# Kernel optimization log

Measured on AMD Instinct MI355X. Metric: run time of the kernel, lower is better.

Reference implementation:

```python
import jax, jax.numpy as jnp
import numpy as np

B, C, T = 32, 512, 2048
OUT_SEQ_LEN = 80
SIGMA2 = 10.0


def setup_inputs() -> dict:
    key = jax.random.key(0)
    k1, k2, k3, k4, k5, k6 = jax.random.split(key, 6)
    x = jax.random.normal(k1, (B, C, T), dtype=jnp.float32)
    # lengths in [T//2, T], with at least one equal to T (torch broadcast assumes max(len)==T)
    len_fea = jax.random.randint(k2, (B,), T // 2, T + 1)
    len_fea = len_fea.at[0].set(T)
    s1 = 1.0 / np.sqrt(C)
    conv1_w = jax.random.uniform(k3, (C, C), jnp.float32, -s1, s1)   # 1x1 conv == linear [out,in]
    conv1_b = jax.random.uniform(k4, (C,), jnp.float32, -s1, s1)
    conv2_w = jax.random.uniform(k5, (C,), jnp.float32, -s1, s1)     # out_channels=1, squeezed
    conv2_b = jax.random.uniform(k6, (), jnp.float32, -s1, s1)
    return {"x": x, "len_fea": len_fea, "conv1_w": conv1_w, "conv1_b": conv1_b,
            "conv2_w": conv2_w, "conv2_b": conv2_b}


def reference(x, len_fea, conv1_w, conv1_b, conv2_w, conv2_b):
    b_size, _, Tt = x.shape
    unaligned = x  # [B,C,T]
    h = jax.nn.relu(x)
    h = jnp.einsum('oc,bct->bot', conv1_w, h) + conv1_b[None, :, None]  # 1x1 conv
    h = jax.nn.relu(h)
    g = jnp.einsum('c,bct->bt', conv2_w, h) + conv2_b                   # 1x1 conv to 1 channel
    g = jax.nn.sigmoid(g)                                               # rec=True path
    gls_ends = jnp.cumsum(g, axis=1)            # [B,T]
    gls_centers = gls_ends - g * 0.5            # [B,T]
    aligned_lengths = gls_ends[jnp.arange(b_size), len_fea - 1]         # [B]
    out_pos = 0.5 + jnp.arange(OUT_SEQ_LEN, dtype=x.dtype)              # rec=True positions
    w = gls_centers[:, None, :] - out_pos[None, :, None]                # [B,L,T]
    w = -(w * w) / SIGMA2
    mask = (jnp.arange(Tt)[None, :] >= len_fea[:, None]).astype(x.dtype)  # [B,T]
    w = w - 1e9 * mask[:, None, :]
    w = jax.nn.softmax(w, axis=-1)
    aligned_features = jnp.einsum('blt,bct->blc', w, unaligned)         # [B,L,C]
    return aligned_features, aligned_lengths
```

## Files before the change

### kernel.cpp

```cpp
#include <hip/hip_runtime.h>
#include <hip/hip_bf16.h>

#define NB 32
#define NC 512
#define NT 2048
#define NL 80
static constexpr float kInvSigma2 = 0.1f;

typedef __attribute__((ext_vector_type(8))) __bf16 bf16x8;
typedef __attribute__((ext_vector_type(4))) float f32x4;

__global__ __launch_bounds__(256) void k_w1p(const float* __restrict__ w1,
                                             __hip_bfloat16* __restrict__ w1p) {
  const int q = blockIdx.x * 256 + threadIdx.x;
  const int c_lo = (q & 3) << 3;
  const int o_lo = (q >> 2) & 15;
  const int c5 = (q >> 6) & 15;
  const int o4 = q >> 10;
  const int o = (o4 << 4) + o_lo;
  const int c = (c5 << 5) + c_lo;
  const float4 p0 = *reinterpret_cast<const float4*>(&w1[o * NC + c]);
  const float4 p1 = *reinterpret_cast<const float4*>(&w1[o * NC + c + 4]);
  bf16x8 v;
  v[0] = (__bf16)p0.x; v[1] = (__bf16)p0.y;
  v[2] = (__bf16)p0.z; v[3] = (__bf16)p0.w;
  v[4] = (__bf16)p1.x; v[5] = (__bf16)p1.y;
  v[6] = (__bf16)p1.z; v[7] = (__bf16)p1.w;
  *reinterpret_cast<bf16x8*>(&w1p[(size_t)q * 8]) = v;
}

__global__ __launch_bounds__(512, 4) void k_g_mfma(
    const float* __restrict__ x, const __hip_bfloat16* __restrict__ w1p,
    const float* __restrict__ b1, const float* __restrict__ w2,
    const float* __restrict__ b2, float* __restrict__ g) {
  __shared__ __hip_bfloat16 bs[64 * 512];
  __shared__ float pws[8][64];
  const int blk = blockIdx.x;
  const int b = blk >> 5;
  const int t0 = (blk & 31) << 6;
  const int tid = threadIdx.x;
  const int w = tid >> 6;
  const int lane = tid & 63;
  const int ln = tid & 15;
  const int kg = lane >> 4;
  const int ob = w << 6;

  const int tl = (tid & 15) << 2;
  const int cp = (tid >> 4) << 1;
  const float* xb = x + (size_t)b * NC * NT + t0;

  auto wr_pair = [&](int t, int c, float lo_f, float hi_f) {
    const __hip_bfloat16 lo = __float2bfloat16(fmaxf(lo_f, 0.f));
    const __hip_bfloat16 hi = __float2bfloat16(fmaxf(hi_f, 0.f));
    const unsigned pk =
        ((unsigned)*reinterpret_cast<const unsigned short*>(&hi) << 16) |
        *reinterpret_cast<const unsigned short*>(&lo);
    const int gran = ((c >> 3) ^ (t & 7) ^ ((t >> 3) & 7)) & 7;
    const int base = (c >> 3) & ~7;
    *reinterpret_cast<unsigned*>(
        (char*)bs + (t << 10) + (((base | gran) << 4) | ((c & 7) << 1))) = pk;
  };

#pragma unroll
  for (int i = 0; i < 4; ++i) {
    const int c = (i << 6) + cp;
    const float4 va = *reinterpret_cast<const float4*>(&xb[(size_t)c * NT + tl]);
    const float4 vb =
        *reinterpret_cast<const float4*>(&xb[(size_t)(c + 1) * NT + tl]);
    const float fa[4] = {va.x, va.y, va.z, va.w};
    const float fb[4] = {vb.x, vb.y, vb.z, vb.w};
#pragma unroll
    for (int j = 0; j < 4; ++j) wr_pair(tl + j, c, fa[j], fb[j]);
  }
  __syncthreads();

  float4 ha[4], hb[4];
#pragma unroll
  for (int i = 0; i < 4; ++i) {
    const int c = 256 + (i << 6) + cp;
    ha[i] = *reinterpret_cast<const float4*>(&xb[(size_t)c * NT + tl]);
    hb[i] = *reinterpret_cast<const float4*>(&xb[(size_t)(c + 1) * NT + tl]);
  }

  f32x4 acc[4][4];
#pragma unroll
  for (int ot = 0; ot < 4; ++ot)
#pragma unroll
    for (int nt = 0; nt < 4; ++nt) acc[ot][nt] = (f32x4){0.f, 0.f, 0.f, 0.f};

  int rowb[4], xm[4];
#pragma unroll
  for (int nt = 0; nt < 4; ++nt) {
    const int tr = (nt << 4) + ln;
    rowb[nt] = tr << 10;
    xm[nt] = (((tr & 7) ^ ((tr >> 3) & 7)) & 7) << 4;
  }
  const __hip_bfloat16* abase =
      w1p + ((size_t)w << 15) + (ln << 5) + (kg << 3);
  const char* bsb = (const char*)bs;

  auto kloop = [&](int ks0, int ks1) {
#pragma unroll 4
    for (int ks = ks0; ks < ks1; ++ks) {
      const int gb = (ks << 6) + (kg << 4);
      bf16x8 bfrag[4];
#pragma unroll
      for (int nt = 0; nt < 4; ++nt)
        bfrag[nt] = *reinterpret_cast<const bf16x8*>(
            bsb + rowb[nt] + (gb ^ xm[nt]));
      __builtin_amdgcn_s_setprio(1);
#pragma unroll
      for (int ot = 0; ot < 4; ++ot) {
        const bf16x8 af = *reinterpret_cast<const bf16x8*>(
            abase + (ot << 13) + (ks << 9));
#pragma unroll
        for (int nt = 0; nt < 4; ++nt)
          acc[ot][nt] = __builtin_amdgcn_mfma_f32_16x16x32_bf16(
              af, bfrag[nt], acc[ot][nt], 0, 0, 0);
      }
      __builtin_amdgcn_s_setprio(0);
    }
  };

  kloop(0, 8);

#pragma unroll
  for (int i = 0; i < 4; ++i) {
    const int c = 256 + (i << 6) + cp;
    const float fa[4] = {ha[i].x, ha[i].y, ha[i].z, ha[i].w};
    const float fb[4] = {hb[i].x, hb[i].y, hb[i].z, hb[i].w};
#pragma unroll
    for (int j = 0; j < 4; ++j) wr_pair(tl + j, c, fa[j], fb[j]);
  }
  __syncthreads();

  kloop(8, 16);

  float pl[4] = {0.f, 0.f, 0.f, 0.f};
#pragma unroll
  for (int ot = 0; ot < 4; ++ot) {
    const int o4 = ob + (ot << 4) + (kg << 2);
    const float4 b1v = *reinterpret_cast<const float4*>(&b1[o4]);
    const float4 w2v = *reinterpret_cast<const float4*>(&w2[o4]);
#pragma unroll
    for (int nt = 0; nt < 4; ++nt) {
      pl[nt] = fmaf(w2v.x, fmaxf(acc[ot][nt][0] + b1v.x, 0.f), pl[nt]);
      pl[nt] = fmaf(w2v.y, fmaxf(acc[ot][nt][1] + b1v.y, 0.f), pl[nt]);
      pl[nt] = fmaf(w2v.z, fmaxf(acc[ot][nt][2] + b1v.z, 0.f), pl[nt]);
      pl[nt] = fmaf(w2v.w, fmaxf(acc[ot][nt][3] + b1v.w, 0.f), pl[nt]);
    }
  }
#pragma unroll
  for (int nt = 0; nt < 4; ++nt) {
    pl[nt] += __shfl_xor(pl[nt], 16, 64);
    pl[nt] += __shfl_xor(pl[nt], 32, 64);
  }
  if (kg == 0) {
#pragma unroll
    for (int nt = 0; nt < 4; ++nt) pws[w][(nt << 4) + ln] = pl[nt];
  }
  __syncthreads();
  if (tid < 64) {
    float s = b2[0];
#pragma unroll
    for (int i = 0; i < 8; ++i) s += pws[i][tid];
    g[b * NT + t0 + tid] = 1.f / (1.f + __expf(-s));
  }
}

__global__ __launch_bounds__(256) void k_g_slow(const float* __restrict__ x,
                                                const float* __restrict__ w1,
                                                const float* __restrict__ b1,
                                                const float* __restrict__ w2,
                                                const float* __restrict__ b2,
                                                float* __restrict__ g) {
  __shared__ __hip_bfloat16 xs[NC][64];
  const int blk = blockIdx.x;
  const int b = blk >> 5;
  const int t0 = (blk & 31) << 6;
  const int tid = threadIdx.x;
  {
    const int tl = (tid & 15) << 2;
    const int c0 = tid >> 4;
    for (int c = c0; c < NC; c += 16) {
      const float4 v = *reinterpret_cast<const float4*>(
          &x[((size_t)b * NC + c) * NT + t0 + tl]);
      xs[c][tl + 0] = __float2bfloat16(fmaxf(v.x, 0.f));
      xs[c][tl + 1] = __float2bfloat16(fmaxf(v.y, 0.f));
      xs[c][tl + 2] = __float2bfloat16(fmaxf(v.z, 0.f));
      xs[c][tl + 3] = __float2bfloat16(fmaxf(v.w, 0.f));
    }
  }
  __syncthreads();
  const int og = tid >> 6;
  const int t = tid & 63;
  float gacc = 0.f;
  for (int pass = 0; pass < 16; ++pass) {
    const int o0 = (og << 7) + (pass << 3);
    float h[8];
#pragma unroll
    for (int j = 0; j < 8; ++j) h[j] = b1[o0 + j];
    const float* wrow = w1 + (size_t)o0 * NC;
#pragma unroll 4
    for (int c = 0; c < NC; ++c) {
      const float xv = __bfloat162float(xs[c][t]);
#pragma unroll
      for (int j = 0; j < 8; ++j) h[j] = fmaf(wrow[j * NC + c], xv, h[j]);
    }
    float p = 0.f;
#pragma unroll
    for (int j = 0; j < 8; ++j) p = fmaf(w2[o0 + j], fmaxf(h[j], 0.f), p);
    gacc += p;
  }
  __syncthreads();
  float* gr = reinterpret_cast<float*>(&xs[0][0]);
  gr[og * 64 + t] = gacc;
  __syncthreads();
  if (tid < 64) {
    const float s = gr[tid] + gr[64 + tid] + gr[128 + tid] + gr[192 + tid] + b2[0];
    g[b * NT + t0 + tid] = 1.f / (1.f + __expf(-s));
  }
}

__global__ __launch_bounds__(256) void k_scan(const float* __restrict__ g,
                                              const int* __restrict__ len_fea,
                                              float* __restrict__ centers,
                                              float* __restrict__ out_len) {
  const int b = blockIdx.x;
  const int tid = threadIdx.x;
  const float* gb = g + b * NT;
  float v[8];
  {
    const float4 p0 = *reinterpret_cast<const float4*>(&gb[tid * 8]);
    const float4 p1 = *reinterpret_cast<const float4*>(&gb[tid * 8 + 4]);
    v[0] = p0.x; v[1] = p0.y; v[2] = p0.z; v[3] = p0.w;
    v[4] = p1.x; v[5] = p1.y; v[6] = p1.z; v[7] = p1.w;
  }
  float s = 0.f;
#pragma unroll
  for (int j = 0; j < 8; ++j) s += v[j];
  float wscan = s;
  const int lane = tid & 63, wid = tid >> 6;
#pragma unroll
  for (int off = 1; off < 64; off <<= 1) {
    const float o = __shfl_up(wscan, (unsigned)off, 64);
    if (lane >= off) wscan += o;
  }
  __shared__ float wsum[4];
  if (lane == 63) wsum[wid] = wscan;
  __syncthreads();
  float base = 0.f;
#pragma unroll
  for (int i = 0; i < 4; ++i)
    if (i < wid) base += wsum[i];
  float run = base + wscan - s;
  const int li = len_fea[b] - 1;
#pragma unroll
  for (int j = 0; j < 8; ++j) {
    const int t = tid * 8 + j;
    run += v[j];
    centers[b * NT + t] = run - 0.5f * v[j];
    if (t == li) out_len[b] = run;
  }
}

__global__ __launch_bounds__(256) void k_wstats(
    const float* __restrict__ centers, const int* __restrict__ len_fea,
    __hip_bfloat16* __restrict__ wbf) {
  const int b = blockIdx.x / NL;
  const int l = blockIdx.x % NL;
  const int tid = threadIdx.x;
  const int len = len_fea[b];
  const float pos = 0.5f + (float)l;
  const float* cb = centers + b * NT;
  const int t0 = tid * 8;

  float cv[8];
  {
    const float4 p0 = *reinterpret_cast<const float4*>(&cb[t0]);
    const float4 p1 = *reinterpret_cast<const float4*>(&cb[t0 + 4]);
    cv[0] = p0.x; cv[1] = p0.y; cv[2] = p0.z; cv[3] = p0.w;
    cv[4] = p1.x; cv[5] = p1.y; cv[6] = p1.z; cv[7] = p1.w;
  }
  float lg[8];
  float m = -3.0e38f;
#pragma unroll
  for (int j = 0; j < 8; ++j) {
    if (t0 + j < len) {
      const float d = cv[j] - pos;
      lg[j] = -d * d * kInvSigma2;
      m = fmaxf(m, lg[j]);
    } else {
      lg[j] = -3.0e38f;
    }
  }
  const int lane = tid & 63, wid = tid >> 6;
#pragma unroll
  for (int off = 32; off > 0; off >>= 1) m = fmaxf(m, __shfl_xor(m, off, 64));
  __shared__ float redm[4];
  if (lane == 0) redm[wid] = m;
  __syncthreads();
  const float M = fmaxf(fmaxf(redm[0], redm[1]), fmaxf(redm[2], redm[3]));

  float e[8];
  float ssum = 0.f;
#pragma unroll
  for (int j = 0; j < 8; ++j) {
    e[j] = (t0 + j < len) ? __expf(lg[j] - M) : 0.f;
    ssum += e[j];
  }
#pragma unroll
  for (int off = 32; off > 0; off >>= 1) ssum += __shfl_xor(ssum, off, 64);
  __shared__ float reds[4];
  if (lane == 0) reds[wid] = ssum;
  __syncthreads();
  const float rinv = 1.f / (reds[0] + reds[1] + reds[2] + reds[3]);

  bf16x8 o;
#pragma unroll
  for (int j = 0; j < 8; ++j) o[j] = (__bf16)(e[j] * rinv);
  *reinterpret_cast<bf16x8*>(&wbf[((size_t)b * NL + l) * NT + t0]) = o;
}

__global__ __launch_bounds__(256) void k_out_mfma(
    const float* __restrict__ x, const __hip_bfloat16* __restrict__ wbf,
    float* __restrict__ out) {
  __shared__ float red[3][64][41];
  const int blk = blockIdx.x;
  const int b = blk >> 4;
  const int c0 = (blk & 15) << 5;
  const int tid = threadIdx.x;
  const int w = tid >> 6;
  const int lane = tid & 63;
  const int ln = tid & 15;
  const int kg = lane >> 4;
  const int tbase = w << 9;

  f32x4 acc[5][2];
#pragma unroll
  for (int lt = 0; lt < 5; ++lt)
#pragma unroll
    for (int nt = 0; nt < 2; ++nt) acc[lt][nt] = (f32x4){0.f, 0.f, 0.f, 0.f};

  const __hip_bfloat16* abase =
      wbf + ((size_t)b * NL + ln) * NT + tbase + (kg << 3);
  const float* bbase = x + ((size_t)b * NC + c0 + ln) * NT + tbase + (kg << 3);

#pragma unroll 4
  for (int ks = 0; ks < 16; ++ks) {
    const int ck = ks << 5;
    bf16x8 bfrag[2];
#pragma unroll
    for (int nt = 0; nt < 2; ++nt) {
      const float4 p0 =
          *reinterpret_cast<const float4*>(bbase + nt * 16 * NT + ck);
      const float4 p1 =
          *reinterpret_cast<const float4*>(bbase + nt * 16 * NT + ck + 4);
      bf16x8 v;
      v[0] = (__bf16)p0.x; v[1] = (__bf16)p0.y;
      v[2] = (__bf16)p0.z; v[3] = (__bf16)p0.w;
      v[4] = (__bf16)p1.x; v[5] = (__bf16)p1.y;
      v[6] = (__bf16)p1.z; v[7] = (__bf16)p1.w;
      bfrag[nt] = v;
    }
#pragma unroll
    for (int lt = 0; lt < 5; ++lt) {
      const bf16x8 af =
          *reinterpret_cast<const bf16x8*>(abase + lt * 16 * NT + ck);
      acc[lt][0] = __builtin_amdgcn_mfma_f32_16x16x32_bf16(af, bfrag[0],
                                                           acc[lt][0], 0, 0, 0);
      acc[lt][1] = __builtin_amdgcn_mfma_f32_16x16x32_bf16(af, bfrag[1],
                                                           acc[lt][1], 0, 0, 0);
    }
  }

  if (w > 0) {
#pragma unroll
    for (int lt = 0; lt < 5; ++lt)
#pragma unroll
      for (int nt = 0; nt < 2; ++nt)
#pragma unroll
        for (int j = 0; j < 4; ++j)
          red[w - 1][lane][lt * 8 + nt * 4 + j] = acc[lt][nt][j];
  }
  __syncthreads();
  if (w == 0) {
#pragma unroll
    for (int lt = 0; lt < 5; ++lt)
#pragma unroll
      for (int nt = 0; nt < 2; ++nt)
#pragma unroll
        for (int j = 0; j < 4; ++j) {
          float s = acc[lt][nt][j];
#pragma unroll
          for (int i = 0; i < 3; ++i) s += red[i][lane][lt * 8 + nt * 4 + j];
          const int l = lt * 16 + (kg << 2) + j;
          out[((size_t)b * NL + l) * NC + c0 + nt * 16 + ln] = s;
        }
  }
}

__global__ __launch_bounds__(256) void k_stats(const float* __restrict__ centers,
                                               const int* __restrict__ len_fea,
                                               float* __restrict__ rmax,
                                               float* __restrict__ rinv) {
  const int b = blockIdx.x / NL;
  const int l = blockIdx.x % NL;
  const int tid = threadIdx.x;
  const int len = len_fea[b];
  const float pos = 0.5f + (float)l;
  const float* cb = centers + b * NT;
  float lg[8];
  float m = -3.0e38f;
  const int t0 = tid * 8;
#pragma unroll
  for (int j = 0; j < 8; ++j) {
    const int t = t0 + j;
    if (t < len) {
      const float d = cb[t] - pos;
      lg[j] = -d * d * kInvSigma2;
      m = fmaxf(m, lg[j]);
    } else {
      lg[j] = -3.0e38f;
    }
  }
  const int lane = tid & 63, wid = tid >> 6;
#pragma unroll
  for (int off = 32; off > 0; off >>= 1) m = fmaxf(m, __shfl_xor(m, off, 64));
  __shared__ float redm[4];
  if (lane == 0) redm[wid] = m;
  __syncthreads();
  const float M = fmaxf(fmaxf(redm[0], redm[1]), fmaxf(redm[2], redm[3]));
  float ssum = 0.f;
#pragma unroll
  for (int j = 0; j < 8; ++j) {
    if (t0 + j < len) ssum += __expf(lg[j] - M);
  }
#pragma unroll
  for (int off = 32; off > 0; off >>= 1) ssum += __shfl_xor(ssum, off, 64);
  __shared__ float reds[4];
  if (lane == 0) reds[wid] = ssum;
  __syncthreads();
  if (tid == 0) {
    const float S = reds[0] + reds[1] + reds[2] + reds[3];
    rmax[blockIdx.x] = M;
    rinv[blockIdx.x] = 1.f / S;
  }
}

__global__ __launch_bounds__(128) void k_out(const float* __restrict__ x,
                                             const int* __restrict__ len_fea,
                                             const float* __restrict__ centers,
                                             const float* __restrict__ rmax,
                                             const float* __restrict__ rinv,
                                             float* __restrict__ out) {
  __shared__ float xsh[128][65];
  __shared__ float wsh[20][64];
  const int blk = blockIdx.x;
  const int b = blk >> 4;
  const int l0 = ((blk >> 2) & 3) * 20;
  const int c0 = (blk & 3) * 128;
  const int tid = threadIdx.x;
  const int len = len_fea[b];
  float acc[20];
#pragma unroll
  for (int l = 0; l < 20; ++l) acc[l] = 0.f;

  for (int t0 = 0; t0 < NT; t0 += 64) {
    __syncthreads();
    {
      const int tl = (tid & 15) << 2;
      const int r0 = tid >> 4;
      for (int r = r0; r < 128; r += 8) {
        const float4 v = *reinterpret_cast<const float4*>(
            &x[((size_t)b * NC + c0 + r) * NT + t0 + tl]);
        float* p = &xsh[r][tl];
        p[0] = v.x; p[1] = v.y; p[2] = v.z; p[3] = v.w;
      }
    }
#pragma unroll
    for (int k = 0; k < 10; ++k) {
      const int idx = k * 128 + tid;
      const int l = idx >> 6;
      const int tt = idx & 63;
      float wv = 0.f;
      if (t0 + tt < len) {
        const float d = centers[b * NT + t0 + tt] - (0.5f + (float)(l0 + l));
        wv = __expf(-d * d * kInvSigma2 - rmax[b * NL + l0 + l]) *
             rinv[b * NL + l0 + l];
      }
      wsh[l][tt] = wv;
    }
    __syncthreads();
#pragma unroll 4
    for (int tt = 0; tt < 64; ++tt) {
      const float xv = xsh[tid][tt];
#pragma unroll
      for (int l = 0; l < 20; ++l) acc[l] = fmaf(wsh[l][tt], xv, acc[l]);
    }
  }
#pragma unroll
  for (int l = 0; l < 20; ++l)
    out[((size_t)b * NL + l0 + l) * NC + c0 + tid] = acc[l];
}

extern "C" void kernel_launch(void* const* d_in, const int* in_sizes, int n_in,
                              void* d_out, int out_size, void* d_ws, size_t ws_size,
                              hipStream_t stream) {
  const float* x = (const float*)d_in[0];
  const int* len_fea = (const int*)d_in[1];
  const float* w1 = (const float*)d_in[2];
  const float* b1 = (const float*)d_in[3];
  const float* w2 = (const float*)d_in[4];
  const float* b2 = (const float*)d_in[5];

  float* out = (float*)d_out;
  float* out_len = out + (size_t)NB * NL * NC;

  float* ws = (float*)d_ws;
  float* g = ws;
  float* centers = ws + NB * NT;
  float* rmax = ws + 2 * NB * NT;
  float* rinv = rmax + NB * NL;
  __hip_bfloat16* w1p = (__hip_bfloat16*)(rinv + NB * NL);
  __hip_bfloat16* wbf = w1p + (size_t)NC * NC;

  const size_t need_mid = (size_t)(2 * NB * NT + 2 * NB * NL) * 4 +
                          (size_t)NC * NC * 2;
  const size_t need_full = need_mid + (size_t)NB * NL * NT * 2;

  if (ws_size >= need_full) {
    k_w1p<<<(NC * NC) / 2048, 256, 0, stream>>>(w1, w1p);
    k_g_mfma<<<NB * 32, 512, 0, stream>>>(x, w1p, b1, w2, b2, g);
    k_scan<<<NB, 256, 0, stream>>>(g, len_fea, centers, out_len);
    k_wstats<<<NB * NL, 256, 0, stream>>>(centers, len_fea, wbf);
    k_out_mfma<<<NB * 16, 256, 0, stream>>>(x, wbf, out);
  } else if (ws_size >= need_mid) {
    k_w1p<<<(NC * NC) / 2048, 256, 0, stream>>>(w1, w1p);
    k_g_mfma<<<NB * 32, 512, 0, stream>>>(x, w1p, b1, w2, b2, g);
    k_scan<<<NB, 256, 0, stream>>>(g, len_fea, centers, out_len);
    k_stats<<<NB * NL, 256, 0, stream>>>(centers, len_fea, rmax, rinv);
    k_out<<<NB * 16, 128, 0, stream>>>(x, len_fea, centers, rmax, rinv, out);
  } else {
    k_g_slow<<<NB * 32, 256, 0, stream>>>(x, w1, b1, w2, b2, g);
    k_scan<<<NB, 256, 0, stream>>>(g, len_fea, centers, out_len);
    k_stats<<<NB * NL, 256, 0, stream>>>(centers, len_fea, rmax, rinv);
    k_out<<<NB * 16, 128, 0, stream>>>(x, len_fea, centers, rmax, rinv, out);
  }
}
```

Baseline: 122.7 us.

## Stream x into LDS in eight double-buffered chunks interleaved with MFMA steps

The kernel used to stage x in two halves. It loaded 256 channels, synced, then held the second half in registers while the first half of the K-loop ran. Now x is split into eight 64-channel chunks, with two register buffers rotating global loads two chunks ahead. Each chunk's LDS write sits between the two MFMA k-steps of the previous chunk. This is meant to overlap global-load latency with matrix work more finely and to cut the register footprint, at the cost of seven block barriers instead of two.

```diff
diff --git a/kernel.cpp b/kernel.cpp
--- a/kernel.cpp
+++ b/kernel.cpp
@@ -46,7 +46,7 @@
   const int ob = w << 6;
 
   const int tl = (tid & 15) << 2;
-  const int cp = (tid >> 4) << 1;
+  const int cg = tid >> 4;
   const float* xb = x + (size_t)b * NC * NT + t0;
 
   auto wr_pair = [&](int t, int c, float lo_f, float hi_f) {
@@ -61,26 +61,18 @@
         (char*)bs + (t << 10) + (((base | gran) << 4) | ((c & 7) << 1))) = pk;
   };
 
-#pragma unroll
-  for (int i = 0; i < 4; ++i) {
-    const int c = (i << 6) + cp;
-    const float4 va = *reinterpret_cast<const float4*>(&xb[(size_t)c * NT + tl]);
-    const float4 vb =
-        *reinterpret_cast<const float4*>(&xb[(size_t)(c + 1) * NT + tl]);
+  auto issue = [&](int p, float4& va, float4& vb) {
+    const int c = (p << 6) + (cg << 1);
+    va = *reinterpret_cast<const float4*>(&xb[(size_t)c * NT + tl]);
+    vb = *reinterpret_cast<const float4*>(&xb[(size_t)(c + 1) * NT + tl]);
+  };
+  auto writeChunk = [&](int p, const float4& va, const float4& vb) {
+    const int c = (p << 6) + (cg << 1);
     const float fa[4] = {va.x, va.y, va.z, va.w};
     const float fb[4] = {vb.x, vb.y, vb.z, vb.w};
 #pragma unroll
     for (int j = 0; j < 4; ++j) wr_pair(tl + j, c, fa[j], fb[j]);
-  }
-  __syncthreads();
-
-  float4 ha[4], hb[4];
-#pragma unroll
-  for (int i = 0; i < 4; ++i) {
-    const int c = 256 + (i << 6) + cp;
-    ha[i] = *reinterpret_cast<const float4*>(&xb[(size_t)c * NT + tl]);
-    hb[i] = *reinterpret_cast<const float4*>(&xb[(size_t)(c + 1) * NT + tl]);
-  }
+  };
 
   f32x4 acc[4][4];
 #pragma unroll
@@ -99,42 +91,46 @@
       w1p + ((size_t)w << 15) + (ln << 5) + (kg << 3);
   const char* bsb = (const char*)bs;
 
-  auto kloop = [&](int ks0, int ks1) {
-#pragma unroll 4
-    for (int ks = ks0; ks < ks1; ++ks) {
-      const int gb = (ks << 6) + (kg << 4);
-      bf16x8 bfrag[4];
+  auto kstep = [&](int ks) {
+    const int gb = (ks << 6) + (kg << 4);
+    bf16x8 bfrag[4];
+#pragma unroll
+    for (int nt = 0; nt < 4; ++nt)
+      bfrag[nt] = *reinterpret_cast<const bf16x8*>(
+          bsb + rowb[nt] + (gb ^ xm[nt]));
+    __builtin_amdgcn_s_setprio(1);
+#pragma unroll
+    for (int ot = 0; ot < 4; ++ot) {
+      const bf16x8 af = *reinterpret_cast<const bf16x8*>(
+          abase + (ot << 13) + (ks << 9));
 #pragma unroll
       for (int nt = 0; nt < 4; ++nt)
-        bfrag[nt] = *reinterpret_cast<const bf16x8*>(
-            bsb + rowb[nt] + (gb ^ xm[nt]));
-      __builtin_amdgcn_s_setprio(1);
-#pragma unroll
-      for (int ot = 0; ot < 4; ++ot) {
-        const bf16x8 af = *reinterpret_cast<const bf16x8*>(
-            abase + (ot << 13) + (ks << 9));
-#pragma unroll
-        for (int nt = 0; nt < 4; ++nt)
-          acc[ot][nt] = __builtin_amdgcn_mfma_f32_16x16x32_bf16(
-              af, bfrag[nt], acc[ot][nt], 0, 0, 0);
-      }
-      __builtin_amdgcn_s_setprio(0);
-    }
+        acc[ot][nt] = __builtin_amdgcn_mfma_f32_16x16x32_bf16(
+            af, bfrag[nt], acc[ot][nt], 0, 0, 0);
+    }
+    __builtin_amdgcn_s_setprio(0);
   };
 
-  kloop(0, 8);
-
-#pragma unroll
-  for (int i = 0; i < 4; ++i) {
-    const int c = 256 + (i << 6) + cp;
-    const float fa[4] = {ha[i].x, ha[i].y, ha[i].z, ha[i].w};
-    const float fb[4] = {hb[i].x, hb[i].y, hb[i].z, hb[i].w};
-#pragma unroll
-    for (int j = 0; j < 4; ++j) wr_pair(tl + j, c, fa[j], fb[j]);
-  }
-  __syncthreads();
-
-  kloop(8, 16);
+  float4 vaA, vbA, vaB, vbB;
+  issue(0, vaA, vbA);
+  issue(1, vaB, vbB);
+  writeChunk(0, vaA, vbA);
+  __syncthreads();
+
+#pragma unroll
+  for (int p = 0; p < 8; ++p) {
+    if (p < 6) {
+      if (p & 1) issue(p + 2, vaB, vbB);
+      else       issue(p + 2, vaA, vbA);
+    }
+    kstep(2 * p);
+    if (p < 7) {
+      if (p & 1) writeChunk(p + 1, vaA, vbA);
+      else       writeChunk(p + 1, vaB, vbB);
+    }
+    kstep(2 * p + 1);
+    if (p < 7) __syncthreads();
+  }
 
   float pl[4] = {0.f, 0.f, 0.f, 0.f};
 #pragma unroll
```

Result: slower. 146.8 us (+19.6%).
